# Kernel optimization log

Measured on AMD Instinct MI355X. Metric: run time of the kernel, lower is better.

Reference implementation:

```python
import jax, jax.numpy as jnp
import numpy as np

N_NODES = 100000


def _mean_agg(x, src, dst, n_nodes):
    # gather neighbor (src) features, segment-sum into destination nodes, divide by in-degree
    summed = jax.ops.segment_sum(x[src], dst, num_segments=n_nodes)  # [N, d]
    deg = jax.ops.segment_sum(jnp.ones_like(dst, dtype=x.dtype), dst, num_segments=n_nodes)
    return summed / jnp.clip(deg, 1.0)[:, None]  # DGL clamps zero in-degree to 1


def _sage_conv(x, src, dst, W_self, W_neigh, b, n_nodes):
    h_neigh = _mean_agg(x, src, dst, n_nodes)
    # DGL SAGEConv(mean): fc_self(h_self) + fc_neigh(h_neigh); single bias
    return x @ W_self + h_neigh @ W_neigh + b


def setup_inputs() -> dict:
    key = jax.random.key(0)
    ks = jax.random.split(key, 8)
    in_f, hid_f, out_f = 64, 64, 16
    n_edges = 1200000
    return {
        "x": jax.random.normal(ks[0], (N_NODES, in_f), dtype=jnp.float32),
        "src": jax.random.randint(ks[1], (n_edges,), 0, N_NODES),
        "dst": jax.random.randint(ks[2], (n_edges,), 0, N_NODES),
        "W1_self": jax.random.normal(ks[3], (in_f, hid_f), dtype=jnp.float32) / np.sqrt(in_f),
        "W1_neigh": jax.random.normal(ks[4], (in_f, hid_f), dtype=jnp.float32) / np.sqrt(in_f),
        "b1": jnp.zeros((hid_f,), dtype=jnp.float32),
        "W2_self": jax.random.normal(ks[5], (hid_f, out_f), dtype=jnp.float32) / np.sqrt(hid_f),
        "W2_neigh": jax.random.normal(ks[6], (hid_f, out_f), dtype=jnp.float32) / np.sqrt(hid_f),
        "b2": jnp.zeros((out_f,), dtype=jnp.float32),
    }


def reference(x, src, dst, W1_self, W1_neigh, b1, W2_self, W2_neigh, b2):
    h = _sage_conv(x, src, dst, W1_self, W1_neigh, b1, N_NODES)
    h = jax.nn.relu(h)
    h = _sage_conv(h, src, dst, W2_self, W2_neigh, b2, N_NODES)
    return h
```

## Files before the change

kernel.cpp:

```cpp
#include <hip/hip_runtime.h>

#define N_NODES 100000
#define N_EDGES 1200000
#define BK 64
#define NB 1563
#define CHUNK_E 4096
#define NBLK_E 293
#define TOT_H (NB * NBLK_E)
#define NSB2 ((TOT_H + 1023) / 1024)
#define CAP 1536
#define ND1 3125

#define OFF_ROWPTR 0
#define OFF_HISTG  401408
#define OFF_BLK2   2234368
#define OFF_PAIRS  2236416
#define OFF_SORTED 7036928
#define OFF_Y1     11837440
#define OFF_H1     24637440

__device__ __forceinline__ unsigned short f2bf(float f) {
    unsigned u = __float_as_uint(f);
    unsigned r = (u + 0x7fffu + ((u >> 16) & 1u)) >> 16;
    return (unsigned short)r;
}

__global__ __launch_bounds__(256) void hist_dense1_kernel(
    const int* __restrict__ dst, int* __restrict__ hist_g,
    const float* __restrict__ x,
    const float* __restrict__ Wn, const float* __restrict__ Ws,
    const float* __restrict__ b,
    unsigned short* __restrict__ y1, float* __restrict__ z1)
{
    __shared__ float sx[32 * 64];
    const int t = threadIdx.x;

    if (blockIdx.x < NBLK_E) {
        int* h = (int*)sx;
        const int e0 = blockIdx.x * CHUNK_E;
        const int e1 = min(e0 + CHUNK_E, N_EDGES);
        for (int i = t; i < NB; i += 256) h[i] = 0;
        __syncthreads();
        for (int e = e0 + t; e < e1; e += 256)
            atomicAdd(&h[dst[e] >> 6], 1);
        __syncthreads();
        for (int i = t; i < NB; i += 256)
            hist_g[i * NBLK_E + blockIdx.x] = h[i];
        return;
    }

    const int bid = blockIdx.x - NBLK_E;
    const int w = t >> 6;
    const int lane = t & 63;
    const int half = w >> 1;
    const int nsub = (w & 1) * 16;
    const int chunk = bid * 32;

    {
        const float4* gx = (const float4*)(x + (size_t)chunk * 64);
        float4* sx4 = (float4*)sx;
        sx4[t] = gx[t];
        sx4[t + 256] = gx[t + 256];
    }

    const float* W = half ? Ws : Wn;
    const float bj = half ? b[lane] : 0.f;

    __syncthreads();

    float acc[16];
#pragma unroll
    for (int m = 0; m < 16; ++m) acc[m] = 0.f;

#pragma unroll 1
    for (int kh = 0; kh < 2; ++kh) {
        float wr[32];
#pragma unroll
        for (int k = 0; k < 32; ++k) wr[k] = W[(kh * 32 + k) * 64 + lane];
#pragma unroll
        for (int m = 0; m < 16; ++m) {
            const float4* xr = (const float4*)(sx + (nsub + m) * 64) + kh * 8;
            float a0 = 0.f, a1 = 0.f, a2 = 0.f, a3 = 0.f;
#pragma unroll
            for (int k4 = 0; k4 < 8; ++k4) {
                float4 v = xr[k4];
                a0 += v.x * wr[4 * k4 + 0];
                a1 += v.y * wr[4 * k4 + 1];
                a2 += v.z * wr[4 * k4 + 2];
                a3 += v.w * wr[4 * k4 + 3];
            }
            acc[m] += (a0 + a1) + (a2 + a3);
        }
    }

#pragma unroll
    for (int m = 0; m < 16; ++m) {
        const float o = acc[m] + bj;
        const size_t gn = (size_t)(chunk + nsub + m);
        if (half) z1[gn * 64 + lane] = o;
        else      y1[gn * 64 + lane] = f2bf(o);
    }
}

__global__ __launch_bounds__(1024) void scan2_blocks_kernel(
    int* __restrict__ hist_g, int* __restrict__ blk2)
{
    __shared__ int s[1024];
    int i = blockIdx.x * 1024 + threadIdx.x;
    int v = (i < TOT_H) ? hist_g[i] : 0;
    s[threadIdx.x] = v;
    __syncthreads();
    for (int off = 1; off < 1024; off <<= 1) {
        int tv = (threadIdx.x >= off) ? s[threadIdx.x - off] : 0;
        __syncthreads();
        s[threadIdx.x] += tv;
        __syncthreads();
    }
    if (i < TOT_H) hist_g[i] = s[threadIdx.x] - v;
    if (threadIdx.x == 1023) blk2[blockIdx.x] = s[1023];
}

__device__ __forceinline__ void local_tops_scan(const int* blk2, int* tops, int t)
{
    int v = (t < NSB2) ? blk2[t] : 0;
    tops[t] = v;
    __syncthreads();
    for (int off = 1; off < 512; off <<= 1) {
        int tv = (t >= off) ? tops[t - off] : 0;
        __syncthreads();
        tops[t] += tv;
        __syncthreads();
    }
    int ex = tops[t] - v;
    __syncthreads();
    tops[t] = ex;
    __syncthreads();
}

__global__ __launch_bounds__(512) void pair_scatter_kernel(
    const int* __restrict__ src, const int* __restrict__ dst,
    const int* __restrict__ hs_scan, const int* __restrict__ blk2,
    unsigned* __restrict__ pairs)
{
    __shared__ int base_s[NB];
    __shared__ int cur_s[NB];
    __shared__ int tops[512];
    const int b = blockIdx.x;
    const int t = threadIdx.x;
    const int e0 = b * CHUNK_E;
    const int e1 = min(e0 + CHUNK_E, N_EDGES);

    local_tops_scan(blk2, tops, t);

    for (int i = t; i < NB; i += 512) {
        int idx = i * NBLK_E + b;
        base_s[i] = hs_scan[idx] + tops[idx >> 10];
        cur_s[i] = 0;
    }
    __syncthreads();
    for (int e = e0 + t; e < e1; e += 512) {
        int d = dst[e];
        int bk = d >> 6;
        int pos = base_s[bk] + atomicAdd(&cur_s[bk], 1);
        pairs[pos] = ((unsigned)src[e] << 6) | (unsigned)(d & 63);
    }
}

__global__ __launch_bounds__(512) void fused_gather1_kernel(
    const unsigned short* __restrict__ y1,
    const unsigned* __restrict__ pairs,
    const int* __restrict__ hs_scan, const int* __restrict__ blk2,
    int* __restrict__ row_ptr, int* __restrict__ sorted_src,
    float* __restrict__ h1)
{
    __shared__ int slist[CAP];
    __shared__ int hist[BK];
    __shared__ int sc[BK];
    __shared__ int cur[BK];
    __shared__ int tops[512];
    const int b = blockIdx.x;
    const int t = threadIdx.x;

    local_tops_scan(blk2, tops, t);

    const int i0 = b * NBLK_E;
    const int start = hs_scan[i0] + tops[i0 >> 10];
    const int end = (b == NB - 1) ? N_EDGES
                    : hs_scan[i0 + NBLK_E] + tops[(i0 + NBLK_E) >> 10];
    const int cnt = end - start;
    const int node0 = b * BK;

    if (t < BK) hist[t] = 0;
    __syncthreads();
    for (int e = start + t; e < end; e += 512)
        atomicAdd(&hist[pairs[e] & 63u], 1);
    __syncthreads();

    int v = (t < BK) ? hist[t] : 0;
    if (t < BK) sc[t] = v;
    __syncthreads();
    for (int off = 1; off < BK; off <<= 1) {
        int tv = (t >= off && t < BK) ? sc[t - off] : 0;
        __syncthreads();
        if (t < BK) sc[t] += tv;
        __syncthreads();
    }
    const int excl = (t < BK) ? sc[t] - v : 0;
    if (t < BK && node0 + t < N_NODES) row_ptr[node0 + t] = start + excl;
    if (b == NB - 1 && t == 0) row_ptr[N_NODES] = N_EDGES;
    if (t < BK) cur[t] = excl;
    __syncthreads();

    const int wv = t >> 6;
    const int lane = t & 63;
    const int sub = lane >> 5;
    const int sl = lane & 31;
    const int eg = sl >> 3;
    const int fl = sl & 7;

    if (cnt <= CAP) {
        for (int e = start + t; e < end; e += 512) {
            unsigned u = pairs[e];
            int p = atomicAdd(&cur[u & 63u], 1);
            slist[p] = (int)(u >> 6);
        }
        __syncthreads();
        for (int i = t; i < cnt; i += 512)
            sorted_src[start + i] = slist[i];
        for (int q = 0; q < 4; ++q) {
            const int node = wv * 8 + q * 2 + sub;
            const int gn = node0 + node;
            if (gn >= N_NODES) break;
            const int o = sc[node] - hist[node];
            const int dg = hist[node];
            float4* hp = (float4*)(h1 + (size_t)gn * 64);
            float4 z;
            if (eg < 2) z = hp[fl * 2 + eg];
            float a0 = 0.f, a1 = 0.f, a2 = 0.f, a3 = 0.f;
            float a4 = 0.f, a5 = 0.f, a6 = 0.f, a7 = 0.f;
            for (int base = 0; base < dg; base += 8) {
                const int i0e = base + eg;
                const int i1e = base + 4 + eg;
                const bool v0 = i0e < dg, v1 = i1e < dg;
                uint4 r0, r1;
                if (v0) {
                    const int s = slist[o + i0e];
                    r0 = ((const uint4*)(y1 + (size_t)s * 64))[fl];
                }
                if (v1) {
                    const int s = slist[o + i1e];
                    r1 = ((const uint4*)(y1 + (size_t)s * 64))[fl];
                }
                if (v0) {
                    a0 += __uint_as_float(r0.x << 16);
                    a1 += __uint_as_float(r0.x & 0xffff0000u);
                    a2 += __uint_as_float(r0.y << 16);
                    a3 += __uint_as_float(r0.y & 0xffff0000u);
                    a4 += __uint_as_float(r0.z << 16);
                    a5 += __uint_as_float(r0.z & 0xffff0000u);
                    a6 += __uint_as_float(r0.w << 16);
                    a7 += __uint_as_float(r0.w & 0xffff0000u);
                }
                if (v1) {
                    a0 += __uint_as_float(r1.x << 16);
                    a1 += __uint_as_float(r1.x & 0xffff0000u);
                    a2 += __uint_as_float(r1.y << 16);
                    a3 += __uint_as_float(r1.y & 0xffff0000u);
                    a4 += __uint_as_float(r1.z << 16);
                    a5 += __uint_as_float(r1.z & 0xffff0000u);
                    a6 += __uint_as_float(r1.w << 16);
                    a7 += __uint_as_float(r1.w & 0xffff0000u);
                }
            }
#pragma unroll
            for (int d = 8; d <= 16; d <<= 1) {
                a0 += __shfl_xor(a0, d); a1 += __shfl_xor(a1, d);
                a2 += __shfl_xor(a2, d); a3 += __shfl_xor(a3, d);
                a4 += __shfl_xor(a4, d); a5 += __shfl_xor(a5, d);
                a6 += __shfl_xor(a6, d); a7 += __shfl_xor(a7, d);
            }
            const float invd = 1.0f / (float)max(dg, 1);
            if (eg == 0) {
                hp[fl * 2] = make_float4(fmaxf(z.x + a0 * invd, 0.f),
                                         fmaxf(z.y + a1 * invd, 0.f),
                                         fmaxf(z.z + a2 * invd, 0.f),
                                         fmaxf(z.w + a3 * invd, 0.f));
            } else if (eg == 1) {
                hp[fl * 2 + 1] = make_float4(fmaxf(z.x + a4 * invd, 0.f),
                                             fmaxf(z.y + a5 * invd, 0.f),
                                             fmaxf(z.z + a6 * invd, 0.f),
                                             fmaxf(z.w + a7 * invd, 0.f));
            }
        }
    } else {
        if (t < BK) cur[t] = start + excl;
        __syncthreads();
        for (int e = start + t; e < end; e += 512) {
            unsigned u = pairs[e];
            int p = atomicAdd(&cur[u & 63u], 1);
            sorted_src[p] = (int)(u >> 6);
        }
        __syncthreads();
        for (int q = 0; q < 4; ++q) {
            const int node = wv * 8 + q * 2 + sub;
            const int gn = node0 + node;
            if (gn >= N_NODES) break;
            const int o = start + sc[node] - hist[node];
            const int dg = hist[node];
            float4* hp = (float4*)(h1 + (size_t)gn * 64);
            float4 z;
            if (eg < 2) z = hp[fl * 2 + eg];
            float a0 = 0.f, a1 = 0.f, a2 = 0.f, a3 = 0.f;
            float a4 = 0.f, a5 = 0.f, a6 = 0.f, a7 = 0.f;
            for (int base = 0; base < dg; base += 4) {
                const int idx = base + eg;
                if (idx < dg) {
                    const int s = sorted_src[o + idx];
                    uint4 raw = ((const uint4*)(y1 + (size_t)s * 64))[fl];
                    a0 += __uint_as_float(raw.x << 16);
                    a1 += __uint_as_float(raw.x & 0xffff0000u);
                    a2 += __uint_as_float(raw.y << 16);
                    a3 += __uint_as_float(raw.y & 0xffff0000u);
                    a4 += __uint_as_float(raw.z << 16);
                    a5 += __uint_as_float(raw.z & 0xffff0000u);
                    a6 += __uint_as_float(raw.w << 16);
                    a7 += __uint_as_float(raw.w & 0xffff0000u);
                }
            }
#pragma unroll
            for (int d = 8; d <= 16; d <<= 1) {
                a0 += __shfl_xor(a0, d); a1 += __shfl_xor(a1, d);
                a2 += __shfl_xor(a2, d); a3 += __shfl_xor(a3, d);
                a4 += __shfl_xor(a4, d); a5 += __shfl_xor(a5, d);
                a6 += __shfl_xor(a6, d); a7 += __shfl_xor(a7, d);
            }
            const float invd = 1.0f / (float)max(dg, 1);
            if (eg == 0) {
                hp[fl * 2] = make_float4(fmaxf(z.x + a0 * invd, 0.f),
                                         fmaxf(z.y + a1 * invd, 0.f),
                                         fmaxf(z.z + a2 * invd, 0.f),
                                         fmaxf(z.w + a3 * invd, 0.f));
            } else if (eg == 1) {
                hp[fl * 2 + 1] = make_float4(fmaxf(z.x + a4 * invd, 0.f),
                                             fmaxf(z.y + a5 * invd, 0.f),
                                             fmaxf(z.z + a6 * invd, 0.f),
                                             fmaxf(z.w + a7 * invd, 0.f));
            }
        }
    }
}

__global__ __launch_bounds__(256) void dense2_kernel(
    const float* __restrict__ h1,
    const float* __restrict__ Wn, const float* __restrict__ Ws,
    const float* __restrict__ b,
    float* __restrict__ y2, float* __restrict__ out)
{
    __shared__ float sx[32 * 68];
    const int t = threadIdx.x;
    const int w = t >> 6;
    const int lane = t & 63;
    const int half = w >> 1;
    const int nsub = (w & 1) * 16;
    const int j = lane & 15;
    const int g = lane >> 4;
    const int chunk = blockIdx.x * 32;

    {
        const float4* gx = (const float4*)(h1 + (size_t)chunk * 64);
        float4* sx4 = (float4*)sx;
        int r0 = t >> 4, c0 = t & 15;
        sx4[r0 * 17 + c0] = gx[t];
        sx4[(r0 + 16) * 17 + c0] = gx[t + 256];
    }

    const float* W = half ? Ws : Wn;
    const float bj = half ? b[j] : 0.f;

    __syncthreads();

    float acc[4] = {0.f, 0.f, 0.f, 0.f};
#pragma unroll 1
    for (int kh = 0; kh < 2; ++kh) {
        float wr[32];
#pragma unroll
        for (int k = 0; k < 32; ++k) wr[k] = W[(kh * 32 + k) * 16 + j];
#pragma unroll
        for (int q = 0; q < 4; ++q) {
            const float4* xr = (const float4*)(sx + (nsub + q * 4 + g) * 68) + kh * 8;
            float a0 = 0.f, a1 = 0.f, a2 = 0.f, a3 = 0.f;
#pragma unroll
            for (int k4 = 0; k4 < 8; ++k4) {
                float4 v = xr[k4];
                a0 += v.x * wr[4 * k4 + 0];
                a1 += v.y * wr[4 * k4 + 1];
                a2 += v.z * wr[4 * k4 + 2];
                a3 += v.w * wr[4 * k4 + 3];
            }
            acc[q] += (a0 + a1) + (a2 + a3);
        }
    }

#pragma unroll
    for (int q = 0; q < 4; ++q) {
        const float o = acc[q] + bj;
        const size_t gn = (size_t)(chunk + nsub + q * 4 + g);
        if (half) out[gn * 16 + j] = o;
        else      y2[gn * 16 + j] = o;
    }
}

__global__ __launch_bounds__(256) void gather2_kernel(
    const float* __restrict__ y2,
    const int* __restrict__ row_ptr,
    const int* __restrict__ sorted_src,
    float* __restrict__ out)
{
    const int wv = threadIdx.x >> 6;
    const int lane = threadIdx.x & 63;
    const int sub = lane >> 4;
    const int sl = lane & 15;
    const int eg = sl >> 2;
    const int fl = sl & 3;

    const int n = blockIdx.x * 16 + wv * 4 + sub;
    const int start = row_ptr[n];
    const int deg = row_ptr[n + 1] - start;

    float4* op = (float4*)(out + (size_t)n * 16);
    float4 z;
    if (eg == 0) z = op[fl];

    float4 acc = make_float4(0.f, 0.f, 0.f, 0.f);
    for (int base = 0; base < deg; base += 16) {
        int eid = 0;
        if (base + sl < deg) eid = sorted_src[start + base + sl];
#pragma unroll
        for (int jj = 0; jj < 16; jj += 4) {
            const int idx = jj + eg;
            const int s = __shfl(eid, sub * 16 + idx);
            if (base + idx < deg) {
                float4 v = ((const float4*)(y2 + (size_t)s * 16))[fl];
                acc.x += v.x; acc.y += v.y; acc.z += v.z; acc.w += v.w;
            }
        }
    }
#pragma unroll
    for (int d = 4; d <= 8; d <<= 1) {
        acc.x += __shfl_xor(acc.x, d); acc.y += __shfl_xor(acc.y, d);
        acc.z += __shfl_xor(acc.z, d); acc.w += __shfl_xor(acc.w, d);
    }
    const float invd = 1.0f / (float)max(deg, 1);
    if (eg == 0) {
        op[fl] = make_float4(z.x + acc.x * invd, z.y + acc.y * invd,
                             z.z + acc.z * invd, z.w + acc.w * invd);
    }
}

extern "C" void kernel_launch(void* const* d_in, const int* in_sizes, int n_in,
                              void* d_out, int out_size, void* d_ws, size_t ws_size,
                              hipStream_t stream) {
    const float* x   = (const float*)d_in[0];
    const int*   src = (const int*)d_in[1];
    const int*   dst = (const int*)d_in[2];
    const float* W1s = (const float*)d_in[3];
    const float* W1n = (const float*)d_in[4];
    const float* b1  = (const float*)d_in[5];
    const float* W2s = (const float*)d_in[6];
    const float* W2n = (const float*)d_in[7];
    const float* b2  = (const float*)d_in[8];
    float* out = (float*)d_out;

    char* ws = (char*)d_ws;
    int* row_ptr    = (int*)(ws + OFF_ROWPTR);
    int* hist_g     = (int*)(ws + OFF_HISTG);
    int* blk2       = (int*)(ws + OFF_BLK2);
    unsigned* pairs = (unsigned*)(ws + OFF_PAIRS);
    int* sorted_src = (int*)(ws + OFF_SORTED);
    unsigned short* y1 = (unsigned short*)(ws + OFF_Y1);
    float* y2       = (float*)(ws + OFF_Y1);
    float* h1       = (float*)(ws + OFF_H1);

    hist_dense1_kernel<<<NBLK_E + ND1, 256, 0, stream>>>(
        dst, hist_g, x, W1n, W1s, b1, y1, h1);
    scan2_blocks_kernel<<<NSB2, 1024, 0, stream>>>(hist_g, blk2);
    pair_scatter_kernel<<<NBLK_E, 512, 0, stream>>>(src, dst, hist_g, blk2, pairs);
    fused_gather1_kernel<<<NB, 512, 0, stream>>>(y1, pairs, hist_g, blk2,
                                                 row_ptr, sorted_src, h1);
    dense2_kernel<<<ND1, 256, 0, stream>>>(h1, W2n, W2s, b2, y2, out);
    gather2_kernel<<<N_NODES / 16, 256, 0, stream>>>(y2, row_ptr, sorted_src, out);
}
```

Measured before the change: 223.6 us.

## Use bf16 MFMA for layer-1 neighbor projection with 64-node dense tiles

The layer-1 dense part of the fused histogram/dense kernel now handles 64 nodes per block instead of 32, halving the dense block count. Two waves compute x@W_neigh with bf16 MFMA 16x16x32 instructions, converting x and W to bf16 on the fly. The other two waves keep the fp32 scalar path for x@W_self, using the full 64-wide K in registers. This is meant to cut ALU time and redundant weight loads, but it adds bf16 rounding on the inputs to the neighbor projection and leaves the work split unevenly between the MFMA waves and the scalar waves.

```diff
diff --git a/kernel.cpp b/kernel.cpp
--- a/kernel.cpp
+++ b/kernel.cpp
@@ -9,7 +9,8 @@
 #define TOT_H (NB * NBLK_E)
 #define NSB2 ((TOT_H + 1023) / 1024)
 #define CAP 1536
-#define ND1 3125
+#define NDD 1563
+#define ND2 3125
 
 #define OFF_ROWPTR 0
 #define OFF_HISTG  401408
@@ -19,6 +20,9 @@
 #define OFF_Y1     11837440
 #define OFF_H1     24637440
 
+typedef __attribute__((ext_vector_type(8))) short short8;
+typedef __attribute__((ext_vector_type(4))) float f32x4;
+
 __device__ __forceinline__ unsigned short f2bf(float f) {
     unsigned u = __float_as_uint(f);
     unsigned r = (u + 0x7fffu + ((u >> 16) & 1u)) >> 16;
@@ -32,7 +36,7 @@
     const float* __restrict__ b,
     unsigned short* __restrict__ y1, float* __restrict__ z1)
 {
-    __shared__ float sx[32 * 64];
+    __shared__ float sx[64 * 64];
     const int t = threadIdx.x;
 
     if (blockIdx.x < NBLK_E) {
@@ -50,55 +54,89 @@
     }
 
     const int bid = blockIdx.x - NBLK_E;
+    const int chunk = bid * 64;
     const int w = t >> 6;
     const int lane = t & 63;
-    const int half = w >> 1;
-    const int nsub = (w & 1) * 16;
-    const int chunk = bid * 32;
 
     {
         const float4* gx = (const float4*)(x + (size_t)chunk * 64);
         float4* sx4 = (float4*)sx;
-        sx4[t] = gx[t];
-        sx4[t + 256] = gx[t + 256];
-    }
-
-    const float* W = half ? Ws : Wn;
-    const float bj = half ? b[lane] : 0.f;
-
-    __syncthreads();
-
-    float acc[16];
-#pragma unroll
-    for (int m = 0; m < 16; ++m) acc[m] = 0.f;
-
+#pragma unroll
+        for (int i = 0; i < 4; ++i) {
+            const int idx = t + i * 256;
+            if (chunk + (idx >> 4) < N_NODES) sx4[idx] = gx[idx];
+        }
+    }
+    __syncthreads();
+
+    if (w >= 2) {
+        const int n0 = (w - 2) * 32;
+        float wr[64];
+#pragma unroll
+        for (int k = 0; k < 64; ++k) wr[k] = Ws[k * 64 + lane];
+        const float bj = b[lane];
 #pragma unroll 1
-    for (int kh = 0; kh < 2; ++kh) {
-        float wr[32];
-#pragma unroll
-        for (int k = 0; k < 32; ++k) wr[k] = W[(kh * 32 + k) * 64 + lane];
-#pragma unroll
-        for (int m = 0; m < 16; ++m) {
-            const float4* xr = (const float4*)(sx + (nsub + m) * 64) + kh * 8;
+        for (int m = 0; m < 32; ++m) {
+            const int gn = chunk + n0 + m;
+            if (gn >= N_NODES) break;
+            const float4* xr = (const float4*)(sx + (n0 + m) * 64);
             float a0 = 0.f, a1 = 0.f, a2 = 0.f, a3 = 0.f;
 #pragma unroll
-            for (int k4 = 0; k4 < 8; ++k4) {
+            for (int k4 = 0; k4 < 16; ++k4) {
                 float4 v = xr[k4];
                 a0 += v.x * wr[4 * k4 + 0];
                 a1 += v.y * wr[4 * k4 + 1];
                 a2 += v.z * wr[4 * k4 + 2];
                 a3 += v.w * wr[4 * k4 + 3];
             }
-            acc[m] += (a0 + a1) + (a2 + a3);
-        }
-    }
-
-#pragma unroll
-    for (int m = 0; m < 16; ++m) {
-        const float o = acc[m] + bj;
-        const size_t gn = (size_t)(chunk + nsub + m);
-        if (half) z1[gn * 64 + lane] = o;
-        else      y1[gn * 64 + lane] = f2bf(o);
+            z1[(size_t)gn * 64 + lane] = (a0 + a1) + (a2 + a3) + bj;
+        }
+    } else {
+        const int n0 = w * 32;
+        if (chunk + n0 < N_NODES) {
+            const int row = lane & 15;
+            const int kg = lane >> 4;
+            short8 bfrag[8];
+#pragma unroll
+            for (int nt = 0; nt < 4; ++nt)
+#pragma unroll
+                for (int kt = 0; kt < 2; ++kt) {
+                    short8 f;
+#pragma unroll
+                    for (int j = 0; j < 8; ++j) {
+                        const int k = kt * 32 + kg * 8 + j;
+                        f[j] = (short)f2bf(Wn[k * 64 + nt * 16 + row]);
+                    }
+                    bfrag[nt * 2 + kt] = f;
+                }
+            f32x4 acc[8];
+#pragma unroll
+            for (int i = 0; i < 8; ++i) acc[i] = (f32x4){0.f, 0.f, 0.f, 0.f};
+#pragma unroll
+            for (int mt = 0; mt < 2; ++mt)
+#pragma unroll
+                for (int kt = 0; kt < 2; ++kt) {
+                    const float* ap = sx + (n0 + mt * 16 + row) * 64 + kt * 32 + kg * 8;
+                    short8 af;
+#pragma unroll
+                    for (int j = 0; j < 8; ++j) af[j] = (short)f2bf(ap[j]);
+#pragma unroll
+                    for (int nt = 0; nt < 4; ++nt)
+                        acc[mt * 4 + nt] = __builtin_amdgcn_mfma_f32_16x16x32_bf16(
+                            af, bfrag[nt * 2 + kt], acc[mt * 4 + nt], 0, 0, 0);
+                }
+#pragma unroll
+            for (int mt = 0; mt < 2; ++mt)
+#pragma unroll
+                for (int nt = 0; nt < 4; ++nt) {
+                    const f32x4 a = acc[mt * 4 + nt];
+#pragma unroll
+                    for (int r = 0; r < 4; ++r) {
+                        const int node = n0 + mt * 16 + 4 * kg + r;
+                        y1[(size_t)(chunk + node) * 64 + nt * 16 + row] = f2bf(a[r]);
+                    }
+                }
+        }
     }
 }
 
@@ -481,12 +519,12 @@
     float* y2       = (float*)(ws + OFF_Y1);
     float* h1       = (float*)(ws + OFF_H1);
 
-    hist_dense1_kernel<<<NBLK_E + ND1, 256, 0, stream>>>(
+    hist_dense1_kernel<<<NBLK_E + NDD, 256, 0, stream>>>(
         dst, hist_g, x, W1n, W1s, b1, y1, h1);
     scan2_blocks_kernel<<<NSB2, 1024, 0, stream>>>(hist_g, blk2);
     pair_scatter_kernel<<<NBLK_E, 512, 0, stream>>>(src, dst, hist_g, blk2, pairs);
     fused_gather1_kernel<<<NB, 512, 0, stream>>>(y1, pairs, hist_g, blk2,
                                                  row_ptr, sorted_src, h1);
-    dense2_kernel<<<ND1, 256, 0, stream>>>(h1, W2n, W2s, b2, y2, out);
+    dense2_kernel<<<ND2, 256, 0, stream>>>(h1, W2n, W2s, b2, y2, out);
     gather2_kernel<<<N_NODES / 16, 256, 0, stream>>>(y2, row_ptr, sorted_src, out);
 }
```

Result: slower. 272.7 us (+21.9%).
